# Kernel tuning notes

Hardware: AMD Instinct MI355X
Metric: run time of the kernel (lower is better)

Reference implementation:

```python
import jax, jax.numpy as jnp
import numpy as np

EMBED_DIM = 768
NUM_HEADS = 12
HEAD_DIM = EMBED_DIM // NUM_HEADS
MAX_REL = 50
B, L = 4, 1024


def setup_inputs() -> dict:
    key = jax.random.key(0)
    ks = jax.random.split(key, 8)
    query = jax.random.normal(ks[0], (B, L, EMBED_DIM), dtype=jnp.float32)
    k_in = jax.random.normal(ks[1], (B, L, EMBED_DIM), dtype=jnp.float32)
    v_in = jax.random.normal(ks[2], (B, L, EMBED_DIM), dtype=jnp.float32)
    # monotone float timestamps per batch (arange fill)
    patch_indices = jnp.arange(B * L, dtype=jnp.float32).reshape(B, L)
    std = 1.0 / np.sqrt(EMBED_DIM)
    in_proj_w = jax.random.normal(ks[3], (3 * EMBED_DIM, EMBED_DIM), dtype=jnp.float32) * std
    in_proj_b = jnp.zeros((3 * EMBED_DIM,), dtype=jnp.float32)
    out_proj_w = jax.random.normal(ks[4], (EMBED_DIM, EMBED_DIM), dtype=jnp.float32) * std
    out_proj_b = jnp.zeros((EMBED_DIM,), dtype=jnp.float32)
    rel_bias = jax.random.truncated_normal(ks[5], -2.0, 2.0, (NUM_HEADS, 2 * MAX_REL + 1), dtype=jnp.float32) * 0.1
    return {"query": query, "key": k_in, "value": v_in, "patch_indices": patch_indices,
            "in_proj_w": in_proj_w, "in_proj_b": in_proj_b,
            "out_proj_w": out_proj_w, "out_proj_b": out_proj_b, "rel_bias": rel_bias}


def _attention(query, patch_indices, in_proj_w, in_proj_b, out_proj_w, out_proj_b, rel_bias):
    Bq, Lq, D = query.shape
    H, hd, M = NUM_HEADS, HEAD_DIM, MAX_REL
    qkv = query @ in_proj_w.T + in_proj_b            # [B,L,3D]
    q, k, v = jnp.split(qkv, 3, axis=-1)
    q = q.reshape(Bq, Lq, H, hd).transpose(0, 2, 1, 3) * (hd ** -0.5)
    k = k.reshape(Bq, Lq, H, hd).transpose(0, 2, 1, 3)
    v = v.reshape(Bq, Lq, H, hd).transpose(0, 2, 1, 3)
    scores = jnp.einsum('bhld,bhmd->bhlm', q, k)     # [B,H,L,L]
    # sequence-position relative bias
    idxs = jnp.arange(Lq)
    rel_pos = jnp.clip(idxs[None, :] - idxs[:, None], -M, M) + M   # [L,L]
    scores = scores + rel_bias[:, rel_pos][None]                   # [1,H,L,L]
    # data-dependent relative-time bias
    deltas = patch_indices[:, 1:] - patch_indices[:, :-1]          # [B,L-1]
    dt = jnp.nanmedian(deltas, axis=1)
    dt = jnp.where(jnp.isfinite(dt) & (dt > 0), dt, 1.0)[:, None, None]
    rel_time = patch_indices[:, :, None] - patch_indices[:, None, :]  # [B,L,L]
    invalid = jnp.isnan(rel_time) | (rel_time < -M) | (rel_time > M)
    rel_time = jnp.where(invalid, 0.0, rel_time)
    rel_idx = (jnp.clip(jnp.round(rel_time / dt), -M, M) + M).astype(jnp.int32)  # [B,L,L]
    bias = jnp.take(rel_bias, rel_idx, axis=1)       # [H,B,L,L]
    scores = scores + jnp.moveaxis(bias, 0, 1)       # [B,H,L,L]
    probs = jax.nn.softmax(scores, axis=-1)
    out = jnp.einsum('bhlm,bhmd->bhld', probs, v)
    out = out.transpose(0, 2, 1, 3).reshape(Bq, Lq, D)
    return out @ out_proj_w.T + out_proj_b


def reference(query, key, value, patch_indices, in_proj_w, in_proj_b, out_proj_w, out_proj_b, rel_bias):
    # NOTE: the original module ignores key/value and builds qkv from query.
    return _attention(query, patch_indices, in_proj_w, in_proj_b, out_proj_w, out_proj_b, rel_bias)
```

## Files before the change

### kernel.cpp

```cpp
#include <hip/hip_runtime.h>
#include <hip/hip_bf16.h>

#define BB 4
#define LL 1024
#define DD 768
#define HH 12
#define HD 64
#define MREL 50
#define NBIAS 101
#define GK 768

#define NEG_INF (-__builtin_inff())

#define QB_F   ((size_t)0)
#define KB_F   ((size_t)1572864)
#define VTB_F  ((size_t)3145728)
#define XBF_F  ((size_t)4718592)
#define WIBF_F ((size_t)6291456)
#define WOBF_F ((size_t)7176192)
#define BIDX_F ((size_t)7471104)
#define DT_F   ((size_t)9568256)

#define NQ4  (BB*LL*DD)
#define NWI4 (3*DD*DD)

typedef __attribute__((ext_vector_type(8)))  short bf16x8;
typedef __attribute__((ext_vector_type(4)))  float f32x4;
typedef __attribute__((ext_vector_type(16))) float f32x16;
typedef __attribute__((ext_vector_type(4)))  unsigned int u32x4;

__device__ __forceinline__ unsigned short f2bf(float f) {
    unsigned u = __float_as_uint(f);
    u += 0x7fffu + ((u >> 16) & 1u);
    return (unsigned short)(u >> 16);
}

__device__ __forceinline__ void gload_lds16(const void* g, void* l) {
    __builtin_amdgcn_global_load_lds(
        (const __attribute__((address_space(1))) void*)g,
        (__attribute__((address_space(3))) void*)l, 16, 0, 0);
}

__global__ __launch_bounds__(256) void prep_kernel(
    const float* __restrict__ patch, float* __restrict__ dt,
    const float* __restrict__ q, const float* __restrict__ wi, const float* __restrict__ wo,
    unsigned short* __restrict__ qd_, unsigned short* __restrict__ wid,
    unsigned short* __restrict__ wod) {
    int tid = threadIdx.x;
    if (blockIdx.x >= 4) {
        int i = ((blockIdx.x - 4) * 256 + tid) * 4;
        const float* src; unsigned short* dst; int off;
        if (i < NQ4)              { src = q;  dst = qd_; off = i; }
        else if (i < NQ4 + NWI4)  { src = wi; dst = wid; off = i - NQ4; }
        else                      { src = wo; dst = wod; off = i - NQ4 - NWI4; }
        float4 v = *(const float4*)&src[off];
        ushort4 o;
        o.x = f2bf(v.x); o.y = f2bf(v.y); o.z = f2bf(v.z); o.w = f2bf(v.w);
        *(ushort4*)&dst[off] = o;
        return;
    }
    __shared__ __align__(16) float del[1024];
    __shared__ __align__(16) unsigned long long key64[1024];
    __shared__ int nvalid;
    __shared__ float acc;
    int b = blockIdx.x;
    if (tid == 0) { nvalid = 0; acc = 0.f; }
    __syncthreads();
    int cnt = 0;
#pragma unroll
    for (int r = 0; r < 4; ++r) {
        int i = tid + r * 256;
        float v = __builtin_nanf("");
        if (i < LL - 1) {
            v = patch[b * LL + i + 1] - patch[b * LL + i];
            if (v == v) ++cnt;
        }
        del[i] = v;
        unsigned bits = (v == v) ? __float_as_uint(v) : 0x7FC00000u;
        unsigned ordk = (bits & 0x80000000u) ? ~bits : (bits | 0x80000000u);
        key64[i] = ((unsigned long long)ordk << 10) | (unsigned)i;
    }
    atomicAdd(&nvalid, cnt);
    __syncthreads();
    int i0 = tid, i1 = tid + 256, i2 = tid + 512, i3 = tid + 768;
    float v0 = del[i0], v1 = del[i1], v2 = del[i2], v3 = del[i3];
    unsigned long long k0 = key64[i0], k1 = key64[i1], k2 = key64[i2], k3 = key64[i3];
    int c0 = 0, c1 = 0, c2 = 0, c3 = 0;
#define CMPK(kx) { unsigned long long _k = (kx); \
    c0 += (_k < k0) ? 1 : 0; c1 += (_k < k1) ? 1 : 0; \
    c2 += (_k < k2) ? 1 : 0; c3 += (_k < k3) ? 1 : 0; }
    for (int j = 0; j < 1024; j += 8) {
        ulonglong2 a = *(const ulonglong2*)&key64[j];
        ulonglong2 bq = *(const ulonglong2*)&key64[j + 2];
        ulonglong2 cq = *(const ulonglong2*)&key64[j + 4];
        ulonglong2 dq = *(const ulonglong2*)&key64[j + 6];
        CMPK(a.x); CMPK(a.y); CMPK(bq.x); CMPK(bq.y);
        CMPK(cq.x); CMPK(cq.y); CMPK(dq.x); CMPK(dq.y);
    }
#undef CMPK
    int n = nvalid;
#define FIN(vr, cr) if (vr == vr) { \
    if (n & 1) { if (cr == n / 2) atomicAdd(&acc, vr); } \
    else { if (cr == n / 2 - 1 || cr == n / 2) atomicAdd(&acc, 0.5f * vr); } }
    FIN(v0, c0); FIN(v1, c1); FIN(v2, c2); FIN(v3, c3);
#undef FIN
    __syncthreads();
    if (tid == 0) {
        float m = acc;
        float res = (n > 0 && m == m && fabsf(m) != __builtin_inff() && m > 0.f) ? m : 1.0f;
        dt[b] = res;
    }
}

__global__ __launch_bounds__(256) void bidx_kernel(const float* __restrict__ patch,
                                                   const float* __restrict__ dtb,
                                                   unsigned short* __restrict__ bidx) {
    int flat = (blockIdx.x * 256 + threadIdx.x) * 8;
    int b = flat >> 20;
    int rem = flat & 1048575;
    int i = rem >> 10;
    int j0 = rem & 1023;
    float pi = patch[b * LL + i];
    float inv_dt = 1.0f / dtb[b];
    float4 pa = *(const float4*)&patch[b * LL + j0];
    float4 pb4 = *(const float4*)&patch[b * LL + j0 + 4];
    unsigned out[4];
#define MK(pj, jofs, dst, shift) { \
    int d = (j0 + jofs) - i; d = d < -MREL ? -MREL : (d > MREL ? MREL : d); \
    float rt = pi - (pj); \
    if (!(rt == rt) || rt < -(float)MREL || rt > (float)MREL) rt = 0.f; \
    float fr = fminf(fmaxf(rintf(rt * inv_dt), -(float)MREL), (float)MREL); \
    unsigned u = (unsigned)(d + MREL) | (((unsigned)((int)fr + MREL)) << 8); \
    dst |= (u << shift); }
    unsigned t;
    t = 0; MK(pa.x, 0, t, 0); MK(pa.y, 1, t, 16); out[0] = t;
    t = 0; MK(pa.z, 2, t, 0); MK(pa.w, 3, t, 16); out[1] = t;
    t = 0; MK(pb4.x, 4, t, 0); MK(pb4.y, 5, t, 16); out[2] = t;
    t = 0; MK(pb4.z, 6, t, 0); MK(pb4.w, 7, t, 16); out[3] = t;
#undef MK
    *(uint4*)&bidx[flat] = *(uint4*)&out[0];
}

#define STAGE_DB(boff, kc)                                                     \
    { _Pragma("unroll") for (int r = 0; r < 2; ++r)                            \
          gload_lds16(Ag + (size_t)(r * 32) * GK + (kc),                       \
                      smem_g + (boff) + r * 2048 + tid * 8);                   \
      _Pragma("unroll") for (int r = 0; r < 4; ++r)                            \
          gload_lds16(Bg + (size_t)(r * 32) * GK + (kc),                       \
                      smem_g + (boff) + 4096 + r * 2048 + tid * 8); }

#define GEMM_DB_MAIN()                                                         \
    __shared__ __align__(16) unsigned short smem_g[24576];                     \
    int tid = threadIdx.x;                                                     \
    int m0 = blockIdx.x << 6, n0 = blockIdx.y << 7;                            \
    int lane = tid & 63, w = tid >> 6;                                         \
    int srow = tid >> 3;                                                       \
    int scol = (((tid & 7) ^ (srow & 7)) << 3);   \
    const unsigned short* Ag = Ab + (size_t)(m0 + srow) * GK + scol;           \
    const unsigned short* Bg = Wb + (size_t)(n0 + srow) * GK + scol;           \
    f32x4 acc[4][2];                                                           \
    _Pragma("unroll") for (int i = 0; i < 4; ++i)                              \
        _Pragma("unroll") for (int j = 0; j < 2; ++j)                          \
            acc[i][j] = (f32x4){0.f, 0.f, 0.f, 0.f};                           \
    int qd_ = lane >> 4, rl = lane & 15, xA = rl & 7;                          \
    int rB = w * 32 + rl;                                                      \
    STAGE_DB(0, 0);                                                            \
    int cur = 0;                                                               \
    for (int t = 0; t < GK / 64; ++t) {                                        \
        __syncthreads();    \
        if (t + 1 < GK / 64) STAGE_DB((cur ^ 1) * 12288, (t + 1) * 64);        \
        int bo = cur * 12288;                                                  \
        const unsigned short* Abl = smem_g + bo;                               \
        const unsigned short* Bbl = smem_g + bo + 4096;                        \
        _Pragma("unroll") for (int ks = 0; ks < 2; ++ks) {                     \
            int cb = ((ks * 4 + qd_) ^ xA) << 3;        \
            bf16x8 af[4], bfr[2];                                              \
            _Pragma("unroll") for (int i = 0; i < 4; ++i)                      \
                af[i] = *(const bf16x8*)&Abl[(rl + i * 16) * 64 + cb];         \
            _Pragma("unroll") for (int j = 0; j < 2; ++j)                      \
                bfr[j] = *(const bf16x8*)&Bbl[(rB + j * 16) * 64 + cb];        \
            _Pragma("unroll") for (int i = 0; i < 4; ++i)                      \
                _Pragma("unroll") for (int j = 0; j < 2; ++j)                  \
                    acc[i][j] = __builtin_amdgcn_mfma_f32_16x16x32_bf16(       \
                        af[i], bfr[j], acc[i][j], 0, 0, 0);                    \
        }                                                                      \
        cur ^= 1;                                                              \
    }                                                                          \
    int colL = lane & 15, rq = lane >> 4;

__global__ __launch_bounds__(256) void qkv_gemm(
    const unsigned short* __restrict__ Ab, const unsigned short* __restrict__ Wb,
    const float* __restrict__ bias,
    unsigned short* __restrict__ qb, unsigned short* __restrict__ kb,
    unsigned short* __restrict__ vtb) {
    GEMM_DB_MAIN();
    int sec = n0 / DD;
    int hh0 = (n0 - sec * DD) >> 6;
    unsigned short* Ts = smem_g;
    __syncthreads();
    if (sec == 2) {
#pragma unroll
        for (int j = 0; j < 2; ++j) {
            int col_t = w * 32 + j * 16 + colL;
            float bn = bias[n0 + col_t];
#pragma unroll
            for (int i = 0; i < 4; ++i) {
                ushort4 o;
                o.x = f2bf(acc[i][j][0] + bn);
                o.y = f2bf(acc[i][j][1] + bn);
                o.z = f2bf(acc[i][j][2] + bn);
                o.w = f2bf(acc[i][j][3] + bn);
                *(ushort4*)&Ts[col_t * 72 + i * 16 + rq * 4] = o;
            }
        }
        __syncthreads();
        int nl = tid >> 1, half = tid & 1;
        int d768 = n0 + nl - 2 * DD;
        int hh = d768 >> 6, dd = d768 & 63;
        int b = m0 >> 10, l0 = (m0 & 1023) + half * 32;
        unsigned short* dst = vtb + (((size_t)b * HH + hh) * HD + dd) * LL + l0;
#pragma unroll
        for (int k = 0; k < 4; ++k)
            *(uint4*)&dst[k * 8] = *(const uint4*)&Ts[nl * 72 + half * 32 + k * 8];
    } else {
        float scale = (sec == 0) ? 0.18033688011112042f : 1.0f;
#pragma unroll
        for (int j = 0; j < 2; ++j) {
            int col_t = w * 32 + j * 16 + colL;
            float bn = bias[n0 + col_t];
#pragma unroll
            for (int i = 0; i < 4; ++i) {
                int row_t = i * 16 + rq * 4;
#pragma unroll
                for (int r = 0; r < 4; ++r)
                    Ts[(row_t + r) * 136 + col_t] = f2bf((acc[i][j][r] + bn) * scale);
            }
        }
        __syncthreads();
        int ml = tid >> 2, q4 = tid & 3;
        int b = (m0 + ml) >> 10, l = (m0 + ml) & 1023;
        unsigned short* dst = (sec == 0 ? qb : kb)
                              + (((size_t)b * HH + hh0 + (q4 >> 1)) * LL + l) * HD
                              + (q4 & 1) * 32;
#pragma unroll
        for (int k = 0; k < 4; ++k)
            *(uint4*)&dst[k * 8] = *(const uint4*)&Ts[ml * 136 + q4 * 32 + k * 8];
    }
}

__global__ __launch_bounds__(256) void out_gemm(
    const unsigned short* __restrict__ Ab, const unsigned short* __restrict__ Wb,
    const float* __restrict__ bias, float* __restrict__ C) {
    GEMM_DB_MAIN();
#pragma unroll
    for (int j = 0; j < 2; ++j) {
        int n = n0 + w * 32 + j * 16 + colL;
        float bn = bias[n];
#pragma unroll
        for (int i = 0; i < 4; ++i) {
            int rowb = m0 + i * 16 + rq * 4;
#pragma unroll
            for (int r = 0; r < 4; ++r)
                C[(size_t)(rowb + r) * DD + n] = acc[i][j][r] + bn;
        }
    }
}

__global__ __launch_bounds__(256) void attn_kernel(
    const unsigned short* __restrict__ QB, const unsigned short* __restrict__ KB,
    const unsigned short* __restrict__ VTB, const unsigned short* __restrict__ BIDX,
    const float* __restrict__ relb, unsigned short* __restrict__ aout) {
    __shared__ __align__(16) unsigned short kls[2][64 * 64];
    __shared__ __align__(16) unsigned short vls[2][64 * 64];
    __shared__ float sb[NBIAS];
    __shared__ float psum_s[128];
    __shared__ float linv_s[64];
    float* fcomb = (float*)kls;

    int tid = threadIdx.x;
    int w = tid >> 6, lane = tid & 63, li = lane & 31, qd = lane >> 5;
    int jt = w & 1, it = w >> 1;
    int bh = blockIdx.x, b = bh / HH, h = bh - b * HH;
    int q0 = blockIdx.y << 6;
    if (tid < NBIAS) sb[tid] = relb[h * NBIAS + tid] * 1.44269504088896340736f;
    int i_loc = it * 32 + li;
    int i_abs = q0 + i_loc;
    bf16x8 kq[4];
    const unsigned short* qrow = QB + ((size_t)bh * LL + i_abs) * HD + qd * 8;
#pragma unroll
    for (int ks = 0; ks < 4; ++ks) kq[ks] = *(const bf16x8*)(qrow + ks * 16);
    float l_run = 0.f;
    f32x16 O0, O1;
#pragma unroll
    for (int r = 0; r < 16; ++r) { O0[r] = 0.f; O1[r] = 0.f; }

    int srow = tid >> 3;
    int swc = ((tid & 7) ^ (srow & 7)) << 3;
    const unsigned short* kgb = KB + (size_t)bh * LL * HD;
    const unsigned short* vgb = VTB + (size_t)bh * HD * LL;
    const unsigned short* bxptr = BIDX + ((size_t)b << 20) + (size_t)(q0 + i_loc) * 1024
                                  + jt * 32 + qd * 4;
    int xr = li & 7;

#define STAGE_KV(T, bufi)                                                      \
    { _Pragma("unroll") for (int c = 0; c < 2; ++c)                            \
          gload_lds16(kgb + (size_t)((T) * 64 + c * 32 + srow) * HD + swc,     \
                      &kls[bufi][c * 2048 + tid * 8]);                         \
      _Pragma("unroll") for (int c = 0; c < 2; ++c)                            \
          gload_lds16(vgb + (size_t)(c * 32 + srow) * LL + (T) * 64 + swc,     \
                      &vls[bufi][c * 2048 + tid * 8]); }

    STAGE_KV(0, 0);
    __syncthreads();
    float sb0 = sb[0], sb100 = sb[100];

    for (int kt = 0; kt < 16; ++kt) {
        int cur = kt & 1;
        if (kt + 1 < 16) STAGE_KV(kt + 1, cur ^ 1);
        ushort4 bi0 = *(const ushort4*)(bxptr);
        ushort4 bi1 = *(const ushort4*)(bxptr + 8);
        ushort4 bi2 = *(const ushort4*)(bxptr + 16);
        ushort4 bi3 = *(const ushort4*)(bxptr + 24);
        bxptr += 64;
        f32x16 st;
#pragma unroll
        for (int r = 0; r < 16; ++r) st[r] = 0.f;
#pragma unroll
        for (int ks = 0; ks < 4; ++ks) {
            bf16x8 ak = *(const bf16x8*)&kls[cur][(jt * 32 + li) * 64
                                                 + (((2 * ks + qd) ^ xr) << 3)];
            st = __builtin_amdgcn_mfma_f32_32x32x16_bf16(ak, kq[ks], st, 0, 0, 0);
        }
        int delta = (kt << 6) + (jt << 5) - q0 - (it << 5);
        if (delta >= 81 || delta <= -81) {
            float db = (delta >= 81) ? sb100 : sb0;
#pragma unroll
            for (int g4 = 0; g4 < 4; ++g4) {
                ushort4 bi = (g4 == 0) ? bi0 : (g4 == 1) ? bi1 : (g4 == 2) ? bi2 : bi3;
#pragma unroll
                for (int q = 0; q < 4; ++q) {
                    int r = g4 * 4 + q;
                    unsigned u = (q == 0) ? bi.x : (q == 1) ? bi.y : (q == 2) ? bi.z : bi.w;
                    st[r] = st[r] + db + sb[u >> 8];
                }
            }
        } else {
#pragma unroll
            for (int g4 = 0; g4 < 4; ++g4) {
                ushort4 bi = (g4 == 0) ? bi0 : (g4 == 1) ? bi1 : (g4 == 2) ? bi2 : bi3;
#pragma unroll
                for (int q = 0; q < 4; ++q) {
                    int r = g4 * 4 + q;
                    unsigned u = (q == 0) ? bi.x : (q == 1) ? bi.y : (q == 2) ? bi.z : bi.w;
                    st[r] = st[r] + sb[u & 0xffu] + sb[u >> 8];
                }
            }
        }
        float rs = 0.f;
        unsigned W[8];
#pragma unroll
        for (int pr = 0; pr < 8; ++pr) {
            float p0 = __builtin_amdgcn_exp2f(st[2 * pr]);
            float p1 = __builtin_amdgcn_exp2f(st[2 * pr + 1]);
            rs += p0 + p1;
            unsigned wpk;
            asm("v_cvt_pk_bf16_f32 %0, %1, %2" : "=v"(wpk) : "v"(p0), "v"(p1));
            W[pr] = wpk;
        }
        rs += __shfl_xor(rs, 32);
        l_run += rs;
        auto s02 = __builtin_amdgcn_permlane32_swap(W[0], W[2], false, false);
        auto s13 = __builtin_amdgcn_permlane32_swap(W[1], W[3], false, false);
        auto s46 = __builtin_amdgcn_permlane32_swap(W[4], W[6], false, false);
        auto s57 = __builtin_amdgcn_permlane32_swap(W[5], W[7], false, false);
        u32x4 a0w = {(unsigned)s02[0], (unsigned)s13[0], (unsigned)s02[1], (unsigned)s13[1]};
        u32x4 a1w = {(unsigned)s46[0], (unsigned)s57[0], (unsigned)s46[1], (unsigned)s57[1]};
        bf16x8 ap0 = __builtin_bit_cast(bf16x8, a0w);
        bf16x8 ap1 = __builtin_bit_cast(bf16x8, a1w);
        {
            bf16x8 bv;
            bv = *(const bf16x8*)&vls[cur][li * 64 + (((jt * 4 + qd) ^ xr) << 3)];
            O0 = __builtin_amdgcn_mfma_f32_32x32x16_bf16(ap0, bv, O0, 0, 0, 0);
            bv = *(const bf16x8*)&vls[cur][li * 64 + (((jt * 4 + 2 + qd) ^ xr) << 3)];
            O0 = __builtin_amdgcn_mfma_f32_32x32x16_bf16(ap1, bv, O0, 0, 0, 0);
            bv = *(const bf16x8*)&vls[cur][(32 + li) * 64 + (((jt * 4 + qd) ^ xr) << 3)];
            O1 = __builtin_amdgcn_mfma_f32_32x32x16_bf16(ap0, bv, O1, 0, 0, 0);
            bv = *(const bf16x8*)&vls[cur][(32 + li) * 64 + (((jt * 4 + 2 + qd) ^ xr) << 3)];
            O1 = __builtin_amdgcn_mfma_f32_32x32x16_bf16(ap1, bv, O1, 0, 0, 0);
        }
        __syncthreads();
    }
#undef STAGE_KV
    if (qd == 0) psum_s[jt * 64 + i_loc] = l_run;
    __syncthreads();
    if (jt == 0 && qd == 0)
        linv_s[i_loc] = 1.0f / (psum_s[i_loc] + psum_s[64 + i_loc]);
    if (jt == 1) {
        int ibase = it * 32;
#pragma unroll
        for (int r = 0; r < 16; ++r) {
            int irow = (r & 3) + ((r >> 2) << 3) + (qd << 2);
            fcomb[(ibase + irow) * 64 + li] = O0[r];
            fcomb[(ibase + irow) * 64 + 32 + li] = O1[r];
        }
    }
    __syncthreads();
    if (jt == 0) {
        int ibase = it * 32;
#pragma unroll
        for (int r = 0; r < 16; ++r) {
            int irow = (r & 3) + ((r >> 2) << 3) + (qd << 2);
            float inv = linv_s[ibase + irow];
            float v0 = (O0[r] + fcomb[(ibase + irow) * 64 + li]) * inv;
            float v1 = (O1[r] + fcomb[(ibase + irow) * 64 + 32 + li]) * inv;
            size_t rowoff = (size_t)(b * LL + q0 + ibase + irow) * DD + h * HD;
            aout[rowoff + li] = f2bf(v0);
            aout[rowoff + 32 + li] = f2bf(v1);
        }
    }
}

extern "C" void kernel_launch(void* const* d_in, const int* in_sizes, int n_in,
                              void* d_out, int out_size, void* d_ws, size_t ws_size,
                              hipStream_t stream) {
    const float* query    = (const float*)d_in[0];
    const float* patch    = (const float*)d_in[3];
    const float* in_w     = (const float*)d_in[4];
    const float* in_b     = (const float*)d_in[5];
    const float* out_w    = (const float*)d_in[6];
    const float* out_b    = (const float*)d_in[7];
    const float* rel_bias = (const float*)d_in[8];
    float* ws  = (float*)d_ws;
    float* out = (float*)d_out;

    unsigned short* qb   = (unsigned short*)(ws + QB_F);
    unsigned short* kb   = (unsigned short*)(ws + KB_F);
    unsigned short* vtb  = (unsigned short*)(ws + VTB_F);
    unsigned short* xbf  = (unsigned short*)(ws + XBF_F);
    unsigned short* wibf = (unsigned short*)(ws + WIBF_F);
    unsigned short* wobf = (unsigned short*)(ws + WOBF_F);
    unsigned short* bidx = (unsigned short*)(ws + BIDX_F);

    prep_kernel<<<5380, 256, 0, stream>>>(patch, ws + DT_F, query, in_w, out_w,
                                          xbf, wibf, wobf);
    bidx_kernel<<<2048, 256, 0, stream>>>(patch, ws + DT_F, bidx);
    qkv_gemm<<<dim3(64, 18), 256, 0, stream>>>(xbf, wibf, in_b, qb, kb, vtb);
    attn_kernel<<<dim3(BB * HH, LL / 64), 256, 0, stream>>>(
        qb, kb, vtb, bidx, rel_bias, xbf);
    out_gemm<<<dim3(64, 6), 256, 0, stream>>>(xbf, wobf, out_b, out);
}
```

Before: 194.7 us.

## Double attention query tile to 128 rows with 512-thread blocks sharing K/V

Each attention block now handles 128 query rows with 8 waves instead of 64 rows with 4 waves. The two 4-wave groups share each staged K/V tile, so every thread issues one K load and one V load per stage instead of two of each. The goal is to halve K/V global traffic and staging work per query row. In exchange the grid shrinks to 384 blocks, which lowers block-level parallelism on a large GPU, and the fcomb reduction scratch now spans the whole combined K/V buffer.

Result: slower. 229.9 us (+18.0%).

```diff
diff --git a/kernel.cpp b/kernel.cpp
--- a/kernel.cpp
+++ b/kernel.cpp
@@ -266,24 +266,25 @@
     }
 }
 
-__global__ __launch_bounds__(256) void attn_kernel(
+__global__ __launch_bounds__(512) void attn_kernel(
     const unsigned short* __restrict__ QB, const unsigned short* __restrict__ KB,
     const unsigned short* __restrict__ VTB, const unsigned short* __restrict__ BIDX,
     const float* __restrict__ relb, unsigned short* __restrict__ aout) {
-    __shared__ __align__(16) unsigned short kls[2][64 * 64];
-    __shared__ __align__(16) unsigned short vls[2][64 * 64];
+    __shared__ __align__(16) unsigned short kvls[4][4096];
     __shared__ float sb[NBIAS];
-    __shared__ float psum_s[128];
-    __shared__ float linv_s[64];
-    float* fcomb = (float*)kls;
+    __shared__ float psum_s[256];
+    __shared__ float linv_s[128];
+    float* fcomb = (float*)&kvls[0][0];
 
     int tid = threadIdx.x;
     int w = tid >> 6, lane = tid & 63, li = lane & 31, qd = lane >> 5;
-    int jt = w & 1, it = w >> 1;
+    int qg = w >> 2, wl = w & 3;
+    int jt = wl & 1, it = wl >> 1;
     int bh = blockIdx.x, b = bh / HH, h = bh - b * HH;
-    int q0 = blockIdx.y << 6;
+    int q0 = blockIdx.y << 7;
     if (tid < NBIAS) sb[tid] = relb[h * NBIAS + tid] * 1.44269504088896340736f;
-    int i_loc = it * 32 + li;
+    int il64 = it * 32 + li;
+    int i_loc = qg * 64 + il64;
     int i_abs = q0 + i_loc;
     bf16x8 kq[4];
     const unsigned short* qrow = QB + ((size_t)bh * LL + i_abs) * HD + qd * 8;
@@ -303,12 +304,10 @@
     int xr = li & 7;
 
 #define STAGE_KV(T, bufi)                                                      \
-    { _Pragma("unroll") for (int c = 0; c < 2; ++c)                            \
-          gload_lds16(kgb + (size_t)((T) * 64 + c * 32 + srow) * HD + swc,     \
-                      &kls[bufi][c * 2048 + tid * 8]);                         \
-      _Pragma("unroll") for (int c = 0; c < 2; ++c)                            \
-          gload_lds16(vgb + (size_t)(c * 32 + srow) * LL + (T) * 64 + swc,     \
-                      &vls[bufi][c * 2048 + tid * 8]); }
+    { gload_lds16(kgb + (size_t)((T) * 64 + srow) * HD + swc,                  \
+                  &kvls[bufi][tid * 8]);                                       \
+      gload_lds16(vgb + (size_t)srow * LL + (T) * 64 + swc,                    \
+                  &kvls[2 + bufi][tid * 8]); }
 
     STAGE_KV(0, 0);
     __syncthreads();
@@ -327,11 +326,11 @@
         for (int r = 0; r < 16; ++r) st[r] = 0.f;
 #pragma unroll
         for (int ks = 0; ks < 4; ++ks) {
-            bf16x8 ak = *(const bf16x8*)&kls[cur][(jt * 32 + li) * 64
-                                                 + (((2 * ks + qd) ^ xr) << 3)];
+            bf16x8 ak = *(const bf16x8*)&kvls[cur][(jt * 32 + li) * 64
+                                                  + (((2 * ks + qd) ^ xr) << 3)];
             st = __builtin_amdgcn_mfma_f32_32x32x16_bf16(ak, kq[ks], st, 0, 0, 0);
         }
-        int delta = (kt << 6) + (jt << 5) - q0 - (it << 5);
+        int delta = (kt << 6) + (jt << 5) - q0 - (qg << 6) - (it << 5);
         if (delta >= 81 || delta <= -81) {
             float db = (delta >= 81) ? sb100 : sb0;
 #pragma unroll
@@ -379,29 +378,30 @@
         bf16x8 ap1 = __builtin_bit_cast(bf16x8, a1w);
         {
             bf16x8 bv;
-            bv = *(const bf16x8*)&vls[cur][li * 64 + (((jt * 4 + qd) ^ xr) << 3)];
+            bv = *(const bf16x8*)&kvls[2 + cur][li * 64 + (((jt * 4 + qd) ^ xr) << 3)];
             O0 = __builtin_amdgcn_mfma_f32_32x32x16_bf16(ap0, bv, O0, 0, 0, 0);
-            bv = *(const bf16x8*)&vls[cur][li * 64 + (((jt * 4 + 2 + qd) ^ xr) << 3)];
+            bv = *(const bf16x8*)&kvls[2 + cur][li * 64 + (((jt * 4 + 2 + qd) ^ xr) << 3)];
             O0 = __builtin_amdgcn_mfma_f32_32x32x16_bf16(ap1, bv, O0, 0, 0, 0);
-            bv = *(const bf16x8*)&vls[cur][(32 + li) * 64 + (((jt * 4 + qd) ^ xr) << 3)];
+            bv = *(const bf16x8*)&kvls[2 + cur][(32 + li) * 64 + (((jt * 4 + qd) ^ xr) << 3)];
             O1 = __builtin_amdgcn_mfma_f32_32x32x16_bf16(ap0, bv, O1, 0, 0, 0);
-            bv = *(const bf16x8*)&vls[cur][(32 + li) * 64 + (((jt * 4 + 2 + qd) ^ xr) << 3)];
+            bv = *(const bf16x8*)&kvls[2 + cur][(32 + li) * 64 + (((jt * 4 + 2 + qd) ^ xr) << 3)];
             O1 = __builtin_amdgcn_mfma_f32_32x32x16_bf16(ap1, bv, O1, 0, 0, 0);
         }
         __syncthreads();
     }
 #undef STAGE_KV
-    if (qd == 0) psum_s[jt * 64 + i_loc] = l_run;
+    if (qd == 0) psum_s[qg * 128 + jt * 64 + il64] = l_run;
     __syncthreads();
     if (jt == 0 && qd == 0)
-        linv_s[i_loc] = 1.0f / (psum_s[i_loc] + psum_s[64 + i_loc]);
+        linv_s[qg * 64 + il64] = 1.0f /
+            (psum_s[qg * 128 + il64] + psum_s[qg * 128 + 64 + il64]);
     if (jt == 1) {
         int ibase = it * 32;
 #pragma unroll
         for (int r = 0; r < 16; ++r) {
             int irow = (r & 3) + ((r >> 2) << 3) + (qd << 2);
-            fcomb[(ibase + irow) * 64 + li] = O0[r];
-            fcomb[(ibase + irow) * 64 + 32 + li] = O1[r];
+            fcomb[qg * 4096 + (ibase + irow) * 64 + li] = O0[r];
+            fcomb[qg * 4096 + (ibase + irow) * 64 + 32 + li] = O1[r];
         }
     }
     __syncthreads();
@@ -410,10 +410,10 @@
 #pragma unroll
         for (int r = 0; r < 16; ++r) {
             int irow = (r & 3) + ((r >> 2) << 3) + (qd << 2);
-            float inv = linv_s[ibase + irow];
-            float v0 = (O0[r] + fcomb[(ibase + irow) * 64 + li]) * inv;
-            float v1 = (O1[r] + fcomb[(ibase + irow) * 64 + 32 + li]) * inv;
-            size_t rowoff = (size_t)(b * LL + q0 + ibase + irow) * DD + h * HD;
+            float inv = linv_s[qg * 64 + ibase + irow];
+            float v0 = (O0[r] + fcomb[qg * 4096 + (ibase + irow) * 64 + li]) * inv;
+            float v1 = (O1[r] + fcomb[qg * 4096 + (ibase + irow) * 64 + 32 + li]) * inv;
+            size_t rowoff = (size_t)(b * LL + q0 + qg * 64 + ibase + irow) * DD + h * HD;
             aout[rowoff + li] = f2bf(v0);
             aout[rowoff + 32 + li] = f2bf(v1);
         }
@@ -445,7 +445,7 @@
                                           xbf, wibf, wobf);
     bidx_kernel<<<2048, 256, 0, stream>>>(patch, ws + DT_F, bidx);
     qkv_gemm<<<dim3(64, 18), 256, 0, stream>>>(xbf, wibf, in_b, qb, kb, vtb);
-    attn_kernel<<<dim3(BB * HH, LL / 64), 256, 0, stream>>>(
+    attn_kernel<<<dim3(BB * HH, LL / 128), 512, 0, stream>>>(
         qb, kb, vtb, bidx, rel_bias, xbf);
     out_gemm<<<dim3(64, 6), 256, 0, stream>>>(xbf, wobf, out_b, out);
 }
```
